# Optimization experiments

Hardware: AMD Instinct MI355X
Metric: run time of the kernel (lower is better)

Reference implementation:

```python
import jax, jax.numpy as jnp
import numpy as np

DIM, H, M = 1024, 8, 512
DH = DIM // H


def setup_inputs() -> dict:
    key = jax.random.key(0)
    k1, k2 = jax.random.split(key)
    z = jax.random.normal(k1, (8, 4096, DIM), dtype=jnp.float32)
    codebook = jax.random.normal(k2, (H, M, DH), dtype=jnp.float32) * 0.02
    return {"z": z, "codebook": codebook}


def reference(z, codebook):
    """Hard straight-through multi-head VQ quantisation.

    z:        [B, L, dim]
    codebook: [H, M, d_head]
    Returns (z_q [B,L,dim], indices [B,L,H], per_head_distances [B,L,H]).
    """
    B, L, _ = z.shape
    z_h = z.reshape(B, L, H, DH)                       # [B,L,H,dh]
    # squared-L2 distances, batched over all heads at once
    z_sq = jnp.sum(z_h * z_h, axis=-1, keepdims=True)  # [B,L,H,1]
    c_sq = jnp.sum(codebook * codebook, axis=-1)       # [H,M]
    cross = jnp.einsum('blhd,hmd->blhm', z_h, codebook)
    dists = jnp.maximum(z_sq + c_sq[None, None] - 2.0 * cross, 0.0)  # [B,L,H,M]
    idx = jnp.argmin(dists, axis=-1)                   # [B,L,H]
    min_d = jnp.take_along_axis(dists, idx[..., None], axis=-1)[..., 0]  # [B,L,H]
    # gather nearest codebook entry per head: codebook[h, idx[b,l,h]]
    e = codebook[jnp.arange(H)[None, None, :], idx]    # [B,L,H,dh]
    # straight-through: forward value = e, gradient = identity to z
    z_q_h = z_h + jax.lax.stop_gradient(e - z_h)
    z_q = z_q_h.reshape(B, L, DIM)
    return z_q, idx, min_d
```

## Files before the change

### kernel.cpp

```cpp
#include <hip/hip_runtime.h>
#include <cfloat>
#include <cstdint>

#define H_    8
#define DH_   128
#define M_    512
#define DIM_  1024
#define BL_   32768

#define BPOS    128
#define THREADS 512
#define NC      128
#define NCHUNK  (M_ / NC)
#define CAP     16
#define EPS     0.02f

typedef _Float16 half8 __attribute__((ext_vector_type(8)));
typedef float floatx4 __attribute__((ext_vector_type(4)));

#define OFF_Z16  0
#define OFF_CB   (OFF_Z16 + 32768)
#define OFF_ZSQ  (OFF_CB + 32768)
#define OFF_CSQ  (OFF_ZSQ + 512)
#define OFF_CNT  (OFF_CSQ + 512)
#define OFF_CI   (OFF_CNT + 512)
#define OFF_WIN  (OFF_CI + 8192)
#define LDS_TOTAL (OFF_WIN + 512)

extern __shared__ char smem[];

__device__ __forceinline__ int swz(int row, int g) { return (g ^ (row & 15)) << 4; }

__device__ __forceinline__ float exact_d(const float* __restrict__ zr,
                                         const float* __restrict__ cr,
                                         float zsq)
{
    float cx0=0,cx1=0,cx2=0,cx3=0,cq0=0,cq1=0,cq2=0,cq3=0;
    #pragma unroll 8
    for (int k4 = 0; k4 < 32; ++k4) {
        float4 a = *(const float4*)(zr + k4 * 4);
        float4 b = *(const float4*)(cr + k4 * 4);
        cx0 = fmaf(a.x, b.x, cx0); cx1 = fmaf(a.y, b.y, cx1);
        cx2 = fmaf(a.z, b.z, cx2); cx3 = fmaf(a.w, b.w, cx3);
        cq0 = fmaf(b.x, b.x, cq0); cq1 = fmaf(b.y, b.y, cq1);
        cq2 = fmaf(b.z, b.z, cq2); cq3 = fmaf(b.w, b.w, cq3);
    }
    float cross = (cx0 + cx1) + (cx2 + cx3);
    float csqe  = (cq0 + cq1) + (cq2 + cq3);
    float d = (zsq + csqe) - 2.0f * cross;
    return fmaxf(d, 0.f);
}

__global__ __launch_bounds__(THREADS, 4) void vq_kernel(
    const float* __restrict__ z,
    const float* __restrict__ cbk,
    float* __restrict__ out_zq,
    float* __restrict__ out_idx,
    float* __restrict__ out_mind)
{
    char*  z16  = smem + OFF_Z16;
    char*  cbB  = smem + OFF_CB;
    float* zsqS = (float*)(smem + OFF_ZSQ);
    float* csqS = (float*)(smem + OFF_CSQ);
    int*   cntS = (int*)(smem + OFF_CNT);
    int*   candI = (int*)(smem + OFF_CI);
    int*   winS  = (int*)(smem + OFF_WIN);

    const int tid   = threadIdx.x;
    const int lane  = tid & 63;
    const int w     = tid >> 6;
    const int bx    = blockIdx.x;
    const int h     = bx & 7;
    const int posBase = (bx >> 3) * BPOS;

    const float* zBlk = z   + (size_t)posBase * DIM_ + h * DH_;
    const float* cbH  = cbk + (size_t)h * M_ * DH_;

    {
        int row = tid >> 2, j = tid & 3;
        const float* zr = zBlk + (size_t)row * DIM_;
        #pragma unroll
        for (int k = 0; k < 4; ++k) {
            int g = j + 4 * k;
            float4 v0 = *(const float4*)(zr + g * 8);
            float4 v1 = *(const float4*)(zr + g * 8 + 4);
            half8 hv;
            hv[0]=(_Float16)v0.x; hv[1]=(_Float16)v0.y; hv[2]=(_Float16)v0.z; hv[3]=(_Float16)v0.w;
            hv[4]=(_Float16)v1.x; hv[5]=(_Float16)v1.y; hv[6]=(_Float16)v1.z; hv[7]=(_Float16)v1.w;
            *(half8*)(z16 + row * 256 + swz(row, g)) = hv;
        }
        if (tid < BPOS) cntS[tid] = 0;
    }

    if (tid < BPOS) {
        const float* zr = zBlk + (size_t)tid * DIM_;
        float ax=0.f, ay=0.f, az=0.f, aw=0.f;
        #pragma unroll
        for (int c4 = 0; c4 < 32; ++c4) {
            float4 v = *(const float4*)(zr + c4 * 4);
            ax = fmaf(v.x, v.x, ax); ay = fmaf(v.y, v.y, ay);
            az = fmaf(v.z, v.z, az); aw = fmaf(v.w, v.w, aw);
        }
        zsqS[tid] = (ax + ay) + (az + aw);
    }

    half8 afr[4];
    float rmin[4] = {FLT_MAX, FLT_MAX, FLT_MAX, FLT_MAX};

    #pragma unroll
    for (int ch = 0; ch < NCHUNK; ++ch) {
        const int mBase = ch * NC;

        {
            int row = tid >> 2, j = tid & 3;
            const float* cr = cbH + (size_t)(mBase + row) * DH_;
            float s = 0.f;
            #pragma unroll
            for (int k = 0; k < 4; ++k) {
                int g = j + 4 * k;
                float4 v0 = *(const float4*)(cr + g * 8);
                float4 v1 = *(const float4*)(cr + g * 8 + 4);
                half8 hv;
                hv[0]=(_Float16)v0.x; hv[1]=(_Float16)v0.y; hv[2]=(_Float16)v0.z; hv[3]=(_Float16)v0.w;
                hv[4]=(_Float16)v1.x; hv[5]=(_Float16)v1.y; hv[6]=(_Float16)v1.z; hv[7]=(_Float16)v1.w;
                *(half8*)(cbB + row * 256 + swz(row, g)) = hv;
                s = fmaf(v0.x, v0.x, s); s = fmaf(v0.y, v0.y, s);
                s = fmaf(v0.z, v0.z, s); s = fmaf(v0.w, v0.w, s);
                s = fmaf(v1.x, v1.x, s); s = fmaf(v1.y, v1.y, s);
                s = fmaf(v1.z, v1.z, s); s = fmaf(v1.w, v1.w, s);
            }
            s += __shfl_xor(s, 1, 4);
            s += __shfl_xor(s, 2, 4);
            if (j == 0) csqS[row] = s;
        }
        __syncthreads();

        if (ch == 0) {
            int row = (w << 4) + (lane & 15);
            #pragma unroll
            for (int ks = 0; ks < 4; ++ks)
                afr[ks] = *(const half8*)(z16 + row * 256 + swz(row, ks * 4 + (lane >> 4)));
        }

        floatx4 acc[8];
        #pragma unroll
        for (int nt = 0; nt < 8; ++nt) acc[nt] = (floatx4){0.f, 0.f, 0.f, 0.f};

        #pragma unroll
        for (int ks = 0; ks < 4; ++ks) {
            int g = ks * 4 + (lane >> 4);
            half8 bn[8];
            #pragma unroll
            for (int nt = 0; nt < 8; ++nt) {
                int crow = nt * 16 + (lane & 15);
                bn[nt] = *(const half8*)(cbB + crow * 256 + swz(crow, g));
            }
            #pragma unroll
            for (int nt = 0; nt < 8; ++nt)
                acc[nt] = __builtin_amdgcn_mfma_f32_16x16x32_f16(afr[ks], bn[nt], acc[nt], 0, 0, 0);
        }

        float cs[8];
        #pragma unroll
        for (int nt = 0; nt < 8; ++nt) cs[nt] = csqS[nt * 16 + (lane & 15)];
        const int colm = mBase + (lane & 15);

        #pragma unroll
        for (int r = 0; r < 4; ++r) {
            float v[8];
            #pragma unroll
            for (int nt = 0; nt < 8; ++nt) v[nt] = fmaf(-2.f, acc[nt][r], cs[nt]);
            float pm = fminf(fminf(fminf(v[0], v[1]), fminf(v[2], v[3])),
                             fminf(fminf(v[4], v[5]), fminf(v[6], v[7])));
            pm = fminf(pm, __shfl_xor(pm, 1, 16));
            pm = fminf(pm, __shfl_xor(pm, 2, 16));
            pm = fminf(pm, __shfl_xor(pm, 4, 16));
            pm = fminf(pm, __shfl_xor(pm, 8, 16));
            rmin[r] = fminf(rmin[r], pm);
            float thr = rmin[r] + EPS;
            int row = (w << 4) + (lane >> 4) * 4 + r;
            #pragma unroll
            for (int nt = 0; nt < 8; ++nt) {
                if (v[nt] <= thr) {
                    int slot = atomicAdd(&cntS[row], 1);
                    if (slot < CAP) candI[row * CAP + slot] = colm + nt * 16;
                }
            }
        }
        if (ch < NCHUNK - 1) __syncthreads();
    }
    __syncthreads();

    {
        int row = tid >> 2, j = tid & 3;
        int cnt = cntS[row];
        float zsq = zsqS[row];
        const float* zr = zBlk + (size_t)row * DIM_;

        float bd = FLT_MAX; int bi = 0x7fffffff;
        if (cnt > CAP) {
            for (int m = j; m < M_; m += 4) {
                float d = exact_d(zr, cbH + (size_t)m * DH_, zsq);
                if (d < bd || (d == bd && m < bi)) { bd = d; bi = m; }
            }
        } else {
            for (int c = j; c < cnt; c += 4) {
                int m = candI[row * CAP + c];
                float d = exact_d(zr, cbH + (size_t)m * DH_, zsq);
                if (d < bd || (d == bd && m < bi)) { bd = d; bi = m; }
            }
        }
        #pragma unroll
        for (int off = 1; off < 4; off <<= 1) {
            float od = __shfl_xor(bd, off, 4);
            int   oi = __shfl_xor(bi, off, 4);
            if (od < bd || (od == bd && oi < bi)) { bd = od; bi = oi; }
        }
        if (j == 0) {
            if (bi < 0 || bi >= M_) bi = 0;
            size_t gp = (size_t)(posBase + row) * H_ + h;
            out_idx[gp]  = (float)bi;
            out_mind[gp] = bd;
            winS[row] = bi;
        }
    }
    __syncthreads();

    #pragma unroll
    for (int it = 0; it < 8; ++it) {
        int gidx = tid + THREADS * it;
        int row = gidx >> 5, c4 = gidx & 31;
        int m = winS[row];
        float4 v = *(const float4*)(cbH + (size_t)m * DH_ + c4 * 4);
        *(float4*)(out_zq + (size_t)(posBase + row) * DIM_ + h * DH_ + c4 * 4) = v;
    }
}

extern "C" void kernel_launch(void* const* d_in, const int* in_sizes, int n_in,
                              void* d_out, int out_size, void* d_ws, size_t ws_size,
                              hipStream_t stream) {
    const float* z   = (const float*)d_in[0];
    const float* cbk = (const float*)d_in[1];

    float* zq    = (float*)d_out;
    float* oidx  = zq + (size_t)BL_ * DIM_;
    float* omind = oidx + (size_t)BL_ * H_;

    hipFuncSetAttribute((const void*)vq_kernel,
                        hipFuncAttributeMaxDynamicSharedMemorySize, LDS_TOTAL);

    dim3 grid((BL_ / BPOS) * H_);
    dim3 block(THREADS);
    hipLaunchKernelGGL(vq_kernel, grid, block, LDS_TOTAL, stream,
                       z, cbk, zq, oidx, omind);
}
```

Baseline: 166.1 us.

## Precompute fp16 swizzled codebook in prep kernel and stream it via global_load_lds

A new prep kernel converts the codebook to fp16 once, in the pre-swizzled LDS layout, and computes codebook squared norms into workspace. The main kernel then copies each codebook chunk straight into LDS with global_load_lds, and loads its z MFMA fragments straight from global memory into registers, which drops the z16 LDS staging area. The goal is to remove the conversion work repeated by every block and to cut LDS use so occupancy can rise (launch bounds go from 4 to 6). The cost is an extra kernel launch and workspace traffic, and codebook norms are now read from global memory on each chunk.

```diff
diff --git a/kernel.cpp b/kernel.cpp
--- a/kernel.cpp
+++ b/kernel.cpp
@@ -18,11 +18,12 @@
 typedef _Float16 half8 __attribute__((ext_vector_type(8)));
 typedef float floatx4 __attribute__((ext_vector_type(4)));
 
-#define OFF_Z16  0
-#define OFF_CB   (OFF_Z16 + 32768)
+#define WS_CB_BYTES (H_ * M_ * DH_ * 2)
+#define WS_CSQ_OFF  WS_CB_BYTES
+
+#define OFF_CB   0
 #define OFF_ZSQ  (OFF_CB + 32768)
-#define OFF_CSQ  (OFF_ZSQ + 512)
-#define OFF_CNT  (OFF_CSQ + 512)
+#define OFF_CNT  (OFF_ZSQ + 512)
 #define OFF_CI   (OFF_CNT + 512)
 #define OFF_WIN  (OFF_CI + 8192)
 #define LDS_TOTAL (OFF_WIN + 512)
@@ -30,6 +31,13 @@
 extern __shared__ char smem[];
 
 __device__ __forceinline__ int swz(int row, int g) { return (g ^ (row & 15)) << 4; }
+
+__device__ __forceinline__ half8 cvt8(float4 a, float4 b) {
+    half8 h;
+    h[0]=(_Float16)a.x; h[1]=(_Float16)a.y; h[2]=(_Float16)a.z; h[3]=(_Float16)a.w;
+    h[4]=(_Float16)b.x; h[5]=(_Float16)b.y; h[6]=(_Float16)b.z; h[7]=(_Float16)b.w;
+    return h;
+}
 
 __device__ __forceinline__ float exact_d(const float* __restrict__ zr,
                                          const float* __restrict__ cr,
@@ -51,17 +59,43 @@
     return fmaxf(d, 0.f);
 }
 
-__global__ __launch_bounds__(THREADS, 4) void vq_kernel(
+__global__ __launch_bounds__(256) void prep_kernel(const float* __restrict__ cbk,
+                                                   half8* __restrict__ cbw,
+                                                   float* __restrict__ csqw)
+{
+    int t = blockIdx.x * 256 + threadIdx.x;
+    int g = t & 15;
+    int row = t >> 4;
+    int gs = g ^ (row & 15);
+    const float* src = cbk + (size_t)row * DH_ + gs * 8;
+    float4 v0 = *(const float4*)src;
+    float4 v1 = *(const float4*)(src + 4);
+    cbw[row * 16 + g] = cvt8(v0, v1);
+
+    if (g == 0) {
+        const float* cr = cbk + (size_t)row * DH_;
+        float ax=0.f, ay=0.f, az=0.f, aw=0.f;
+        #pragma unroll
+        for (int c4 = 0; c4 < 32; ++c4) {
+            float4 v = *(const float4*)(cr + c4 * 4);
+            ax = fmaf(v.x, v.x, ax); ay = fmaf(v.y, v.y, ay);
+            az = fmaf(v.z, v.z, az); aw = fmaf(v.w, v.w, aw);
+        }
+        csqw[row] = (ax + ay) + (az + aw);
+    }
+}
+
+__global__ __launch_bounds__(THREADS, 6) void vq_kernel(
     const float* __restrict__ z,
     const float* __restrict__ cbk,
+    const char*  __restrict__ cbw,
+    const float* __restrict__ csqw,
     float* __restrict__ out_zq,
     float* __restrict__ out_idx,
     float* __restrict__ out_mind)
 {
-    char*  z16  = smem + OFF_Z16;
     char*  cbB  = smem + OFF_CB;
     float* zsqS = (float*)(smem + OFF_ZSQ);
-    float* csqS = (float*)(smem + OFF_CSQ);
     int*   cntS = (int*)(smem + OFF_CNT);
     int*   candI = (int*)(smem + OFF_CI);
     int*   winS  = (int*)(smem + OFF_WIN);
@@ -75,22 +109,10 @@
 
     const float* zBlk = z   + (size_t)posBase * DIM_ + h * DH_;
     const float* cbH  = cbk + (size_t)h * M_ * DH_;
-
-    {
-        int row = tid >> 2, j = tid & 3;
-        const float* zr = zBlk + (size_t)row * DIM_;
-        #pragma unroll
-        for (int k = 0; k < 4; ++k) {
-            int g = j + 4 * k;
-            float4 v0 = *(const float4*)(zr + g * 8);
-            float4 v1 = *(const float4*)(zr + g * 8 + 4);
-            half8 hv;
-            hv[0]=(_Float16)v0.x; hv[1]=(_Float16)v0.y; hv[2]=(_Float16)v0.z; hv[3]=(_Float16)v0.w;
-            hv[4]=(_Float16)v1.x; hv[5]=(_Float16)v1.y; hv[6]=(_Float16)v1.z; hv[7]=(_Float16)v1.w;
-            *(half8*)(z16 + row * 256 + swz(row, g)) = hv;
-        }
-        if (tid < BPOS) cntS[tid] = 0;
-    }
+    const char*  cbWH = cbw + (size_t)h * M_ * 256;
+    const float* csqH = csqw + h * M_;
+
+    if (tid < BPOS) cntS[tid] = 0;
 
     if (tid < BPOS) {
         const float* zr = zBlk + (size_t)tid * DIM_;
@@ -105,6 +127,18 @@
     }
 
     half8 afr[4];
+    {
+        int row = (w << 4) + (lane & 15);
+        const float* zr = zBlk + (size_t)row * DIM_;
+        #pragma unroll
+        for (int ks = 0; ks < 4; ++ks) {
+            int g = ks * 4 + (lane >> 4);
+            float4 v0 = *(const float4*)(zr + g * 8);
+            float4 v1 = *(const float4*)(zr + g * 8 + 4);
+            afr[ks] = cvt8(v0, v1);
+        }
+    }
+
     float rmin[4] = {FLT_MAX, FLT_MAX, FLT_MAX, FLT_MAX};
 
     #pragma unroll
@@ -112,35 +146,17 @@
         const int mBase = ch * NC;
 
         {
-            int row = tid >> 2, j = tid & 3;
-            const float* cr = cbH + (size_t)(mBase + row) * DH_;
-            float s = 0.f;
-            #pragma unroll
-            for (int k = 0; k < 4; ++k) {
-                int g = j + 4 * k;
-                float4 v0 = *(const float4*)(cr + g * 8);
-                float4 v1 = *(const float4*)(cr + g * 8 + 4);
-                half8 hv;
-                hv[0]=(_Float16)v0.x; hv[1]=(_Float16)v0.y; hv[2]=(_Float16)v0.z; hv[3]=(_Float16)v0.w;
-                hv[4]=(_Float16)v1.x; hv[5]=(_Float16)v1.y; hv[6]=(_Float16)v1.z; hv[7]=(_Float16)v1.w;
-                *(half8*)(cbB + row * 256 + swz(row, g)) = hv;
-                s = fmaf(v0.x, v0.x, s); s = fmaf(v0.y, v0.y, s);
-                s = fmaf(v0.z, v0.z, s); s = fmaf(v0.w, v0.w, s);
-                s = fmaf(v1.x, v1.x, s); s = fmaf(v1.y, v1.y, s);
-                s = fmaf(v1.z, v1.z, s); s = fmaf(v1.w, v1.w, s);
-            }
-            s += __shfl_xor(s, 1, 4);
-            s += __shfl_xor(s, 2, 4);
-            if (j == 0) csqS[row] = s;
+            const char* src = cbWH + (size_t)mBase * 256;
+            #pragma unroll
+            for (int it = 0; it < 4; ++it) {
+                int off = (tid + THREADS * it) * 16;
+                __builtin_amdgcn_global_load_lds(
+                    (const __attribute__((address_space(1))) unsigned int*)(src + off),
+                    (__attribute__((address_space(3))) unsigned int*)(cbB + off),
+                    16, 0, 0);
+            }
         }
         __syncthreads();
-
-        if (ch == 0) {
-            int row = (w << 4) + (lane & 15);
-            #pragma unroll
-            for (int ks = 0; ks < 4; ++ks)
-                afr[ks] = *(const half8*)(z16 + row * 256 + swz(row, ks * 4 + (lane >> 4)));
-        }
 
         floatx4 acc[8];
         #pragma unroll
@@ -162,7 +178,7 @@
 
         float cs[8];
         #pragma unroll
-        for (int nt = 0; nt < 8; ++nt) cs[nt] = csqS[nt * 16 + (lane & 15)];
+        for (int nt = 0; nt < 8; ++nt) cs[nt] = csqH[mBase + nt * 16 + (lane & 15)];
         const int colm = mBase + (lane & 15);
 
         #pragma unroll
@@ -187,9 +203,8 @@
                 }
             }
         }
-        if (ch < NCHUNK - 1) __syncthreads();
-    }
-    __syncthreads();
+        __syncthreads();
+    }
 
     {
         int row = tid >> 2, j = tid & 3;
@@ -246,11 +261,14 @@
     float* oidx  = zq + (size_t)BL_ * DIM_;
     float* omind = oidx + (size_t)BL_ * H_;
 
-    hipFuncSetAttribute((const void*)vq_kernel,
-                        hipFuncAttributeMaxDynamicSharedMemorySize, LDS_TOTAL);
+    half8* cbw  = (half8*)d_ws;
+    float* csqw = (float*)((char*)d_ws + WS_CSQ_OFF);
+
+    hipLaunchKernelGGL(prep_kernel, dim3(256), dim3(256), 0, stream,
+                       cbk, cbw, csqw);
 
     dim3 grid((BL_ / BPOS) * H_);
     dim3 block(THREADS);
     hipLaunchKernelGGL(vq_kernel, grid, block, LDS_TOTAL, stream,
-                       z, cbk, zq, oidx, omind);
-}
+                       z, cbk, (const char*)cbw, csqw, zq, oidx, omind);
+}
```

Measured after the change: 190.9 us. 15.0% more time.
